# Optimization experiments

Hardware: AMD Instinct MI355X
Metric: run time of the kernel (lower is better)

## Reference

```python
import jax, jax.numpy as jnp
import numpy as np

K = 32768          # random Fourier features of the integrand
MAX_DEPTH = 4      # fixed unroll depth of the adaptive quadtree


def _f_eval(px, py, w, ax, ay, phi):
    # integrand f(x,y) = sum_k w_k * cos(ax_k x + ay_k y + phi_k)
    theta = px[..., None] * ax + py[..., None] * ay + phi  # (..., K)
    return jnp.cos(theta) @ w


def _simpson_cells(xl, xr, yl, yr, w, ax, ay, phi):
    # 2D Simpson estimate per cell; matches _quad_simpsons2D_mem (center point
    # fp[4] has coefficient 0 in the original formula, so it is skipped).
    mx = (xl + xr) * 0.5
    my = (yl + yr) * 0.5
    px = jnp.stack([xl, mx, xr, xl, xr, xl, mx, xr], axis=-1)  # (N, 8)
    py = jnp.stack([yl, yl, yl, my, my, yr, yr, yr], axis=-1)
    fv = _f_eval(px, py, w, ax, ay, phi)                        # (N, 8)
    hx = jnp.abs(xr - xl)
    hy = jnp.abs(yr - yl)
    return hx * hy / 12.0 * (
        -(fv[..., 0] + fv[..., 2] + fv[..., 5] + fv[..., 7])
        + 4.0 * (fv[..., 1] + fv[..., 3] + fv[..., 4] + fv[..., 6]))


def _split(xl, xr, yl, yr):
    # children in quadrant order q0 (LL), q1 (LR), q2 (UL), q3 (UR), interleaved
    mx = (xl + xr) * 0.5
    my = (yl + yr) * 0.5
    cxl = jnp.stack([xl, mx, xl, mx], -1).reshape(-1)
    cxr = jnp.stack([mx, xr, mx, xr], -1).reshape(-1)
    cyl = jnp.stack([yl, yl, my, my], -1).reshape(-1)
    cyr = jnp.stack([my, my, yr, yr], -1).reshape(-1)
    return cxl, cxr, cyl, cyr


def _adaptive_simpson2d(xa, xb, ya, yb, eps, w, ax, ay, phi):
    xl = jnp.reshape(xa, (1,)); xr = jnp.reshape(xb, (1,))
    yl = jnp.reshape(ya, (1,)); yr = jnp.reshape(yb, (1,))
    bounds = [(xl, xr, yl, yr)]
    S = [_simpson_cells(xl, xr, yl, yr, w, ax, ay, phi)]  # (4**d,) per depth
    wholes = [S[0]]  # 'whole' passed into the asr call for each cell
    for d in range(1, MAX_DEPTH + 1):
        b = _split(*bounds[d - 1])
        bounds.append(b)
        Sd = _simpson_cells(*b, w, ax, ay, phi)
        S.append(Sd)
        W = Sd.reshape(-1, 4)
        # NOTE: original code passes q0 (not q3) as 'whole' for quadrant 3 --
        # this bug is reproduced faithfully.
        wholes.append(jnp.stack([W[:, 0], W[:, 1], W[:, 2], W[:, 0]], -1).reshape(-1))
    val = None
    for d in range(MAX_DEPTH - 1, -1, -1):
        sum_q = S[d + 1].reshape(-1, 4).sum(-1)
        delta = sum_q - wholes[d]
        corrected = sum_q + delta / 15.0
        if d == MAX_DEPTH - 1:
            val = corrected  # truncate recursion at max depth
        else:
            child_sum = val.reshape(-1, 4).sum(-1)
            eps_d = eps / (4.0 ** d)  # eps is quartered at each recursion level
            val = jnp.where(jnp.abs(delta) <= 15.0 * eps_d, corrected, child_sum)
    return val[0]


def setup_inputs() -> dict:
    key = jax.random.key(0)
    k1, k2, k3, k4 = jax.random.split(key, 4)
    w = jax.random.normal(k1, (K,), jnp.float32) / np.float32(np.sqrt(K))
    ax = jax.random.normal(k2, (K,), jnp.float32) * 6.0
    ay = jax.random.normal(k3, (K,), jnp.float32) * 6.0
    phi = jax.random.uniform(k4, (K,), jnp.float32) * np.float32(2.0 * np.pi)
    return {"xa": jnp.float32(0.0), "xb": jnp.float32(1.0),
            "ya": jnp.float32(0.0), "yb": jnp.float32(1.0),
            "eps": jnp.float32(1e-6),
            "w": w, "ax": ax, "ay": ay, "phi": phi}


def reference(xa, xb, ya, yb, eps, w, ax, ay, phi):
    return _adaptive_simpson2d(xa, xb, ya, yb, eps, w, ax, ay, phi)
```

## Files before the change

kernel.cpp:

```cpp
#include <hip/hip_runtime.h>
#include <math.h>

#define KFEAT 32768
#define GRID_N 33
#define NPTS (GRID_N * GRID_N)
#define PTS_PER_BLOCK 8
#define PBLOCKS ((NPTS + PTS_PER_BLOCK - 1) / PTS_PER_BLOCK)
#define SPLITK 8
#define FP_STRIDE 1092
#define FP_GROUPS (FP_STRIDE / 4)

__global__ __launch_bounds__(256) void eval_grid_kernel(
    const float4* __restrict__ w4, const float4* __restrict__ ax4,
    const float4* __restrict__ ay4, const float4* __restrict__ phi4,
    const float* __restrict__ xa_p, const float* __restrict__ xb_p,
    const float* __restrict__ ya_p, const float* __restrict__ yb_p,
    float* __restrict__ Fpart) {
  const int tid = threadIdx.x;
  const int pblk = blockIdx.x;
  const int split = blockIdx.y;
  const float xa = xa_p[0], xb = xb_p[0];
  const float ya = ya_p[0], yb = yb_p[0];
  const float sx = (xb - xa) * (1.0f / 32.0f);
  const float sy = (yb - ya) * (1.0f / 32.0f);

  const int p0 = pblk * PTS_PER_BLOCK;
  float x[PTS_PER_BLOCK], y[PTS_PER_BLOCK];
#pragma unroll
  for (int j = 0; j < PTS_PER_BLOCK; ++j) {
    int p = min(p0 + j, NPTS - 1);
    int gx = p % GRID_N;
    int gy = p / GRID_N;
    x[j] = fmaf((float)gx, sx, xa);
    y[j] = fmaf((float)gy, sy, ya);
  }

  const int base4 = split * ((KFEAT / 4) / SPLITK);
  float4 A[4], B[4], P[4], W[4];
#pragma unroll
  for (int u = 0; u < 4; ++u) {
    const int idx = base4 + tid + 256 * u;
    A[u] = ax4[idx];
    B[u] = ay4[idx];
    P[u] = phi4[idx];
    W[u] = w4[idx];
  }

  float acc[PTS_PER_BLOCK];
#pragma unroll
  for (int j = 0; j < PTS_PER_BLOCK; ++j) acc[j] = 0.0f;

#pragma unroll
  for (int u = 0; u < 4; ++u) {
#pragma unroll
    for (int j = 0; j < PTS_PER_BLOCK; ++j) {
      float t0 = fmaf(A[u].x, x[j], fmaf(B[u].x, y[j], P[u].x));
      float t1 = fmaf(A[u].y, x[j], fmaf(B[u].y, y[j], P[u].y));
      float t2 = fmaf(A[u].z, x[j], fmaf(B[u].z, y[j], P[u].z));
      float t3 = fmaf(A[u].w, x[j], fmaf(B[u].w, y[j], P[u].w));
      float s = fmaf(W[u].x, __cosf(t0), fmaf(W[u].y, __cosf(t1),
                fmaf(W[u].z, __cosf(t2), W[u].w * __cosf(t3))));
      acc[j] += s;
    }
  }

  __shared__ float red[4][PTS_PER_BLOCK];
#pragma unroll
  for (int j = 0; j < PTS_PER_BLOCK; ++j) {
    float v = acc[j];
#pragma unroll
    for (int off = 32; off > 0; off >>= 1) v += __shfl_down(v, off, 64);
    if ((tid & 63) == 0) red[tid >> 6][j] = v;
  }
  __syncthreads();
  if (tid < PTS_PER_BLOCK) {
    const int j = tid;
    float v = red[0][j] + red[1][j] + red[2][j] + red[3][j];
    int p = p0 + j;
    if (p < NPTS) Fpart[split * FP_STRIDE + p] = v;
  }
}

__device__ __forceinline__ int compact_bits(int v, int shift) {
  int r = (v >> shift) & 1;
  r |= ((v >> (shift + 2)) & 1) << 1;
  r |= ((v >> (shift + 4)) & 1) << 2;
  r |= ((v >> (shift + 6)) & 1) << 3;
  return r;
}

__device__ __forceinline__ float simpson_cell(const float* __restrict__ F,
                                              int d, int cell, float hx,
                                              float hy) {
  const int ix = compact_bits(cell, 0);
  const int iy = compact_bits(cell, 1);
  const int s = 5 - d;
  const int h = 1 << (s - 1);
  const int gx0 = ix << s, gx1 = gx0 + h, gx2 = gx0 + 2 * h;
  const int gy0 = iy << s, gy1 = gy0 + h, gy2 = gy0 + 2 * h;
  const float f0 = F[gy0 * GRID_N + gx0];
  const float f1 = F[gy0 * GRID_N + gx1];
  const float f2 = F[gy0 * GRID_N + gx2];
  const float f3 = F[gy1 * GRID_N + gx0];
  const float f4 = F[gy1 * GRID_N + gx2];
  const float f5 = F[gy2 * GRID_N + gx0];
  const float f6 = F[gy2 * GRID_N + gx1];
  const float f7 = F[gy2 * GRID_N + gx2];
  return hx * hy * (1.0f / 12.0f) *
         (-(f0 + f2 + f5 + f7) + 4.0f * (f1 + f3 + f4 + f6));
}

__global__ __launch_bounds__(512) void combine_kernel(
    const float* __restrict__ Fpart, const float* __restrict__ xa_p,
    const float* __restrict__ xb_p, const float* __restrict__ ya_p,
    const float* __restrict__ yb_p, const float* __restrict__ eps_p,
    float* __restrict__ out) {
  __shared__ alignas(16) float Fs[FP_STRIDE];
  __shared__ float S4[256], S3[64], S2[16], S1[4], S0[1];
  __shared__ float val3[64], val2[16], val1[4];
  const int t = threadIdx.x;
  const float xa = *xa_p, xb = *xb_p, ya = *ya_p, yb = *yb_p, eps = *eps_p;
  const float HX = fabsf(xb - xa), HY = fabsf(yb - ya);

  if (t < FP_GROUPS) {
    const float4* Fp4 = (const float4*)Fpart;
    float4 s = make_float4(0.0f, 0.0f, 0.0f, 0.0f);
#pragma unroll
    for (int sp = 0; sp < SPLITK; ++sp) {
      float4 v = Fp4[sp * FP_GROUPS + t];
      s.x += v.x; s.y += v.y; s.z += v.z; s.w += v.w;
    }
    ((float4*)Fs)[t] = s;
  }
  __syncthreads();

  if (t < 256) {
    S4[t] = simpson_cell(Fs, 4, t, HX * 0.0625f, HY * 0.0625f);
    if (t < 64) {
      S3[t] = simpson_cell(Fs, 3, t, HX * 0.125f, HY * 0.125f);
    } else if (t < 80) {
      S2[t - 64] = simpson_cell(Fs, 2, t - 64, HX * 0.25f, HY * 0.25f);
    } else if (t < 84) {
      S1[t - 80] = simpson_cell(Fs, 1, t - 80, HX * 0.5f, HY * 0.5f);
    } else if (t == 84) {
      S0[0] = simpson_cell(Fs, 0, 0, HX, HY);
    }
  }
  __syncthreads();

  if (t < 64) {
    float sumq = ((S4[4 * t] + S4[4 * t + 1]) + S4[4 * t + 2]) + S4[4 * t + 3];
    float whole = ((t & 3) == 3) ? S3[t & ~3] : S3[t];
    float delta = sumq - whole;
    val3[t] = sumq + delta * (1.0f / 15.0f);
  }
  __syncthreads();

  if (t < 16) {
    float sumq = ((S3[4 * t] + S3[4 * t + 1]) + S3[4 * t + 2]) + S3[4 * t + 3];
    float whole = ((t & 3) == 3) ? S2[t & ~3] : S2[t];
    float delta = sumq - whole;
    float corrected = sumq + delta * (1.0f / 15.0f);
    float child =
        ((val3[4 * t] + val3[4 * t + 1]) + val3[4 * t + 2]) + val3[4 * t + 3];
    float eps_d = eps * (1.0f / 16.0f);
    val2[t] = (fabsf(delta) <= 15.0f * eps_d) ? corrected : child;
  }
  __syncthreads();

  if (t < 4) {
    float sumq = ((S2[4 * t] + S2[4 * t + 1]) + S2[4 * t + 2]) + S2[4 * t + 3];
    float whole = ((t & 3) == 3) ? S1[t & ~3] : S1[t];
    float delta = sumq - whole;
    float corrected = sumq + delta * (1.0f / 15.0f);
    float child =
        ((val2[4 * t] + val2[4 * t + 1]) + val2[4 * t + 2]) + val2[4 * t + 3];
    float eps_d = eps * 0.25f;
    val1[t] = (fabsf(delta) <= 15.0f * eps_d) ? corrected : child;
  }
  __syncthreads();

  if (t == 0) {
    float sumq = ((S1[0] + S1[1]) + S1[2]) + S1[3];
    float delta = sumq - S0[0];
    float corrected = sumq + delta * (1.0f / 15.0f);
    float child = ((val1[0] + val1[1]) + val1[2]) + val1[3];
    out[0] = (fabsf(delta) <= 15.0f * eps) ? corrected : child;
  }
}

extern "C" void kernel_launch(void* const* d_in, const int* in_sizes, int n_in,
                              void* d_out, int out_size, void* d_ws,
                              size_t ws_size, hipStream_t stream) {
  const float* xa = (const float*)d_in[0];
  const float* xb = (const float*)d_in[1];
  const float* ya = (const float*)d_in[2];
  const float* yb = (const float*)d_in[3];
  const float* eps = (const float*)d_in[4];
  const float4* w4 = (const float4*)d_in[5];
  const float4* ax4 = (const float4*)d_in[6];
  const float4* ay4 = (const float4*)d_in[7];
  const float4* phi4 = (const float4*)d_in[8];
  float* out = (float*)d_out;
  float* Fpart = (float*)d_ws;

  dim3 grid(PBLOCKS, SPLITK);
  eval_grid_kernel<<<grid, 256, 0, stream>>>(w4, ax4, ay4, phi4, xa, xb, ya,
                                             yb, Fpart);
  combine_kernel<<<1, 512, 0, stream>>>(Fpart, xa, xb, ya, yb, eps, out);
}
```

Before: 18.28 us.

## Parallelize eval over grid points per thread and feature chunks per block with atomics

The grid-evaluation kernel now gives each thread up to five grid points and each block a chunk of sixteen features, read as uniform scalar loads. The old layout gave threads features and blocks grid points, which needed a cross-wave shuffle reduction. Partial sums go through atomicAdd into eight bank rows, which are cleared by a memset before launch. This removes the block reductions and the per-thread float4 feature loads, at the cost of many global atomics (2048 blocks by about 1089 points) and an extra memset on the stream.

```diff
diff --git a/kernel.cpp b/kernel.cpp
--- a/kernel.cpp
+++ b/kernel.cpp
@@ -4,80 +4,73 @@
 #define KFEAT 32768
 #define GRID_N 33
 #define NPTS (GRID_N * GRID_N)
-#define PTS_PER_BLOCK 8
-#define PBLOCKS ((NPTS + PTS_PER_BLOCK - 1) / PTS_PER_BLOCK)
-#define SPLITK 8
+#define NKB 2048
+#define KPB (KFEAT / NKB)
+#define NBANK 8
+#define SPLITK NBANK
 #define FP_STRIDE 1092
 #define FP_GROUPS (FP_STRIDE / 4)
 
+template <int ROWS>
+__device__ __forceinline__ void kloop(int kbase, const float* __restrict__ ax,
+                                      const float* __restrict__ ay,
+                                      const float* __restrict__ phi,
+                                      const float* __restrict__ w,
+                                      const float (&x)[5], const float (&y)[5],
+                                      float (&acc)[5]) {
+#pragma unroll
+  for (int kk = 0; kk < KPB; ++kk) {
+    const float A = ax[kbase + kk];
+    const float B = ay[kbase + kk];
+    const float P = phi[kbase + kk];
+    const float W = w[kbase + kk];
+#pragma unroll
+    for (int j = 0; j < ROWS; ++j) {
+      float th = fmaf(A, x[j], fmaf(B, y[j], P));
+      acc[j] = fmaf(W, __cosf(th), acc[j]);
+    }
+  }
+}
+
 __global__ __launch_bounds__(256) void eval_grid_kernel(
-    const float4* __restrict__ w4, const float4* __restrict__ ax4,
-    const float4* __restrict__ ay4, const float4* __restrict__ phi4,
+    const float* __restrict__ w, const float* __restrict__ ax,
+    const float* __restrict__ ay, const float* __restrict__ phi,
     const float* __restrict__ xa_p, const float* __restrict__ xb_p,
     const float* __restrict__ ya_p, const float* __restrict__ yb_p,
     float* __restrict__ Fpart) {
   const int tid = threadIdx.x;
-  const int pblk = blockIdx.x;
-  const int split = blockIdx.y;
+  const int bank = blockIdx.x & (NBANK - 1);
+  const int kbase = blockIdx.x * KPB;
   const float xa = xa_p[0], xb = xb_p[0];
   const float ya = ya_p[0], yb = yb_p[0];
   const float sx = (xb - xa) * (1.0f / 32.0f);
   const float sy = (yb - ya) * (1.0f / 32.0f);
 
-  const int p0 = pblk * PTS_PER_BLOCK;
-  float x[PTS_PER_BLOCK], y[PTS_PER_BLOCK];
-#pragma unroll
-  for (int j = 0; j < PTS_PER_BLOCK; ++j) {
-    int p = min(p0 + j, NPTS - 1);
-    int gx = p % GRID_N;
-    int gy = p / GRID_N;
+  float x[5], y[5], acc[5];
+#pragma unroll
+  for (int j = 0; j < 5; ++j) {
+    int p = tid + 256 * j;
+    int pc = min(p, NPTS - 1);
+    int gx = pc % GRID_N;
+    int gy = pc / GRID_N;
     x[j] = fmaf((float)gx, sx, xa);
     y[j] = fmaf((float)gy, sy, ya);
-  }
-
-  const int base4 = split * ((KFEAT / 4) / SPLITK);
-  float4 A[4], B[4], P[4], W[4];
-#pragma unroll
-  for (int u = 0; u < 4; ++u) {
-    const int idx = base4 + tid + 256 * u;
-    A[u] = ax4[idx];
-    B[u] = ay4[idx];
-    P[u] = phi4[idx];
-    W[u] = w4[idx];
-  }
-
-  float acc[PTS_PER_BLOCK];
-#pragma unroll
-  for (int j = 0; j < PTS_PER_BLOCK; ++j) acc[j] = 0.0f;
-
-#pragma unroll
-  for (int u = 0; u < 4; ++u) {
-#pragma unroll
-    for (int j = 0; j < PTS_PER_BLOCK; ++j) {
-      float t0 = fmaf(A[u].x, x[j], fmaf(B[u].x, y[j], P[u].x));
-      float t1 = fmaf(A[u].y, x[j], fmaf(B[u].y, y[j], P[u].y));
-      float t2 = fmaf(A[u].z, x[j], fmaf(B[u].z, y[j], P[u].z));
-      float t3 = fmaf(A[u].w, x[j], fmaf(B[u].w, y[j], P[u].w));
-      float s = fmaf(W[u].x, __cosf(t0), fmaf(W[u].y, __cosf(t1),
-                fmaf(W[u].z, __cosf(t2), W[u].w * __cosf(t3))));
-      acc[j] += s;
-    }
-  }
-
-  __shared__ float red[4][PTS_PER_BLOCK];
-#pragma unroll
-  for (int j = 0; j < PTS_PER_BLOCK; ++j) {
-    float v = acc[j];
-#pragma unroll
-    for (int off = 32; off > 0; off >>= 1) v += __shfl_down(v, off, 64);
-    if ((tid & 63) == 0) red[tid >> 6][j] = v;
-  }
-  __syncthreads();
-  if (tid < PTS_PER_BLOCK) {
-    const int j = tid;
-    float v = red[0][j] + red[1][j] + red[2][j] + red[3][j];
-    int p = p0 + j;
-    if (p < NPTS) Fpart[split * FP_STRIDE + p] = v;
+    acc[j] = 0.0f;
+  }
+
+  if (tid < 128) {
+    kloop<5>(kbase, ax, ay, phi, w, x, y, acc);
+  } else {
+    kloop<4>(kbase, ax, ay, phi, w, x, y, acc);
+  }
+
+  float* bankrow = Fpart + bank * FP_STRIDE;
+#pragma unroll
+  for (int j = 0; j < 4; ++j) {
+    atomicAdd(&bankrow[tid + 256 * j], acc[j]);
+  }
+  if (tid + 1024 < NPTS) {
+    atomicAdd(&bankrow[tid + 1024], acc[4]);
   }
 }
 
@@ -197,15 +190,16 @@
   const float* ya = (const float*)d_in[2];
   const float* yb = (const float*)d_in[3];
   const float* eps = (const float*)d_in[4];
-  const float4* w4 = (const float4*)d_in[5];
-  const float4* ax4 = (const float4*)d_in[6];
-  const float4* ay4 = (const float4*)d_in[7];
-  const float4* phi4 = (const float4*)d_in[8];
+  const float* w = (const float*)d_in[5];
+  const float* ax = (const float*)d_in[6];
+  const float* ay = (const float*)d_in[7];
+  const float* phi = (const float*)d_in[8];
   float* out = (float*)d_out;
   float* Fpart = (float*)d_ws;
 
-  dim3 grid(PBLOCKS, SPLITK);
-  eval_grid_kernel<<<grid, 256, 0, stream>>>(w4, ax4, ay4, phi4, xa, xb, ya,
-                                             yb, Fpart);
+  hipMemsetAsync(Fpart, 0, NBANK * FP_STRIDE * sizeof(float), stream);
+
+  eval_grid_kernel<<<NKB, 256, 0, stream>>>(w, ax, ay, phi, xa, xb, ya, yb,
+                                            Fpart);
   combine_kernel<<<1, 512, 0, stream>>>(Fpart, xa, xb, ya, yb, eps, out);
 }
```

Result: slower. 29.37 us (+60.7%).
